# Kernel tuning notes

Measured on AMD Instinct MI355X. Metric: run time of the kernel, lower is better.

The kernel has to match this reference:

```python
import jax, jax.numpy as jnp
import numpy as np

# Init kwargs of DecisionGate
A = 1.0
B = 2.0
THRES = 0.5


def soft_gate(x):
    # 1 / (1 + |x/a|^(2b))
    return 1.0 / (1.0 + jnp.abs(x / A) ** (2.0 * B))


def setup_inputs() -> dict:
    key = jax.random.key(0)
    k1, k2 = jax.random.split(key)
    B_, P_, D_ = 4096, 64, 512
    x = jax.random.normal(k1, (B_, P_), dtype=jnp.float32)
    act = jax.random.normal(k2, (B_, D_), dtype=jnp.float32)
    batch_inds = jnp.arange(B_, dtype=jnp.int64)
    return {"x": x, "act": act, "batch_inds": batch_inds}


def reference(x, act, batch_inds):
    """Faithful dense formulation of DecisionGate.forward.

    The torch module returns (gated_x, dict{node p -> (list of act[b]*g[b,p], list of batch_inds[b])
    for all (b,p) with g[b,p] >= thres}). The variable-length dict is a sparse
    repacking of the dense dispatch tensor below: for node p, its gathered
    activations are dispatched[mask[:, p], p, :] and its batch ids are
    batch_inds[mask[:, p]]. We return (gated_x, mask, dispatched) as the
    fixed-shape, jit-compatible equivalent.
    """
    g = soft_gate(x)                      # [B, P]
    mask = g >= THRES                     # [B, P] bool routing decision
    w = jnp.where(mask, g, 0.0)           # zero out sub-threshold gates
    # dispatched[b, p, :] = act[b] * g[b, p] if routed to node p else 0
    dispatched = w[:, :, None] * act[:, None, :]  # [B, P, D]
    return g, mask, dispatched
```

## Files before the change

kernel.cpp:

```cpp
#include <hip/hip_runtime.h>


constexpr int BATCH = 4096;
constexpr int P = 64;
constexpr int D = 512;
constexpr int PCHUNK = 8;
constexpr int NCHUNK = P / PCHUNK;

typedef float vfloat4 __attribute__((ext_vector_type(4)));

__device__ __forceinline__ float gate_val(float xv) {
    const float x2 = xv * xv;
    const float x4 = x2 * x2;
    return 1.0f / (1.0f + x4);
}

__global__ __launch_bounds__(256, 8)
void decision_gate_kernel(const float* __restrict__ x,
                          const float* __restrict__ act,
                          float* __restrict__ g_out,
                          float* __restrict__ mask_out,
                          float* __restrict__ disp) {
    const int bid  = blockIdx.x;
    const int b    = bid >> 3;
    const int p0   = (bid & (NCHUNK - 1)) * PCHUNK;
    const int t    = threadIdx.x;
    const int d4   = t & 127;
    const int psel = t >> 7;

    if (t < PCHUNK) {
        const float g = gate_val(x[(size_t)b * P + p0 + t]);
        g_out[(size_t)b * P + p0 + t]    = g;
        mask_out[(size_t)b * P + p0 + t] = (g >= 0.5f) ? 1.0f : 0.0f;
    }

    const vfloat4 a = reinterpret_cast<const vfloat4*>(act)[(size_t)b * (D / 4) + d4];

    vfloat4* out = reinterpret_cast<vfloat4*>(disp)
                 + (size_t)b * (P * D / 4)
                 + (size_t)p0 * (D / 4)
                 + d4;

    #pragma unroll
    for (int k = 0; k < 4; ++k) {
        const int p = psel + 2 * k;
        const float g  = gate_val(x[(size_t)b * P + p0 + p]);
        const float wp = (g >= 0.5f) ? g : 0.0f;
        out[(size_t)p * (D / 4)] = a * wp;
    }
}

extern "C" void kernel_launch(void* const* d_in, const int* in_sizes, int n_in,
                              void* d_out, int out_size, void* d_ws, size_t ws_size,
                              hipStream_t stream) {
    const float* x   = (const float*)d_in[0];
    const float* act = (const float*)d_in[1];

    float* out      = (float*)d_out;
    float* g_out    = out;
    float* mask_out = out + (size_t)BATCH * P;
    float* disp     = out + (size_t)2 * BATCH * P;

    decision_gate_kernel<<<BATCH * NCHUNK, 256, 0, stream>>>(x, act, g_out, mask_out, disp);
}
```

Baseline: 530.1 us.

## Use grid-stride persistent launch with nontemporal stores for dispatch output

Replaces the one-block-per-(batch, p-chunk) launch with a fixed grid of 2048 blocks. Each thread walks the flattened dispatch tensor with a grid stride and writes it using nontemporal stores. The gate and mask outputs are now computed with vectorized float4 loads and stores by the first threads. This aims to cut block scheduling overhead and cache pollution from the 512 MB streaming write, at the cost of reloading act and x rows once per iteration instead of reusing them within a block.

```diff
diff --git a/kernel.cpp b/kernel.cpp
--- a/kernel.cpp
+++ b/kernel.cpp
@@ -4,8 +4,12 @@
 constexpr int BATCH = 4096;
 constexpr int P = 64;
 constexpr int D = 512;
-constexpr int PCHUNK = 8;
-constexpr int NCHUNK = P / PCHUNK;
+
+constexpr int NTHR = 256;
+constexpr int NBLK = 2048;
+constexpr int GSTRIDE = NBLK * NTHR;
+constexpr long long NF4 = (long long)BATCH * P * (D / 4);
+constexpr int NITER = (int)(NF4 / GSTRIDE);
 
 typedef float vfloat4 __attribute__((ext_vector_type(4)));
 
@@ -15,38 +19,42 @@
     return 1.0f / (1.0f + x4);
 }
 
-__global__ __launch_bounds__(256, 8)
+__global__ __launch_bounds__(NTHR)
 void decision_gate_kernel(const float* __restrict__ x,
                           const float* __restrict__ act,
                           float* __restrict__ g_out,
                           float* __restrict__ mask_out,
                           float* __restrict__ disp) {
-    const int bid  = blockIdx.x;
-    const int b    = bid >> 3;
-    const int p0   = (bid & (NCHUNK - 1)) * PCHUNK;
-    const int t    = threadIdx.x;
-    const int d4   = t & 127;
-    const int psel = t >> 7;
+    const int gid = blockIdx.x * NTHR + threadIdx.x;
 
-    if (t < PCHUNK) {
-        const float g = gate_val(x[(size_t)b * P + p0 + t]);
-        g_out[(size_t)b * P + p0 + t]    = g;
-        mask_out[(size_t)b * P + p0 + t] = (g >= 0.5f) ? 1.0f : 0.0f;
+    if (gid < (BATCH * P) / 4) {
+        const vfloat4 xv = reinterpret_cast<const vfloat4*>(x)[gid];
+        vfloat4 gv, mv;
+        #pragma unroll
+        for (int i = 0; i < 4; ++i) {
+            const float g = gate_val(xv[i]);
+            gv[i] = g;
+            mv[i] = (g >= 0.5f) ? 1.0f : 0.0f;
+        }
+        reinterpret_cast<vfloat4*>(g_out)[gid]    = gv;
+        reinterpret_cast<vfloat4*>(mask_out)[gid] = mv;
     }
 
-    const vfloat4 a = reinterpret_cast<const vfloat4*>(act)[(size_t)b * (D / 4) + d4];
+    const int b0 = gid >> 13;
+    const int p  = (gid >> 7) & (P - 1);
+    const int d4 = gid & (D / 4 - 1);
 
-    vfloat4* out = reinterpret_cast<vfloat4*>(disp)
-                 + (size_t)b * (P * D / 4)
-                 + (size_t)p0 * (D / 4)
-                 + d4;
+    const vfloat4* __restrict__ actv = reinterpret_cast<const vfloat4*>(act);
+    vfloat4* __restrict__ dispv      = reinterpret_cast<vfloat4*>(disp);
 
-    #pragma unroll
-    for (int k = 0; k < 4; ++k) {
-        const int p = psel + 2 * k;
-        const float g  = gate_val(x[(size_t)b * P + p0 + p]);
+    #pragma unroll 4
+    for (int it = 0; it < NITER; ++it) {
+        const int b = b0 + 64 * it;
+        const float xv = x[b * P + p];
+        const float g  = gate_val(xv);
         const float wp = (g >= 0.5f) ? g : 0.0f;
-        out[(size_t)p * (D / 4)] = a * wp;
+        const vfloat4 v = actv[b * (D / 4) + d4] * wp;
+        __builtin_nontemporal_store(v, &dispv[(size_t)gid + (size_t)it * GSTRIDE]);
     }
 }
 
@@ -61,5 +69,5 @@
     float* mask_out = out + (size_t)BATCH * P;
     float* disp     = out + (size_t)2 * BATCH * P;
 
-    decision_gate_kernel<<<BATCH * NCHUNK, 256, 0, stream>>>(x, act, g_out, mask_out, disp);
+    decision_gate_kernel<<<NBLK, NTHR, 0, stream>>>(x, act, g_out, mask_out, disp);
 }
```

New measurement: 560.6 us. 5.8% more time.
